# Performance work log

Hardware: AMD Instinct MI355X
Metric: run time of the kernel (lower is better)

Reference implementation:

```python
import jax, jax.numpy as jnp
import numpy as np

ALPHA = 2.0   # ATan surrogate alpha (spikingjelly default)
VTH = 0.5     # v_threshold
NUM_HEADS = 8

@jax.custom_vjp
def atan_spike(x):
    return (x >= 0.0).astype(x.dtype)

def _atan_fwd(x):
    return atan_spike(x), x

def _atan_bwd(x, g):
    return (g * (ALPHA / 2.0) / (1.0 + (jnp.pi / 2.0 * ALPHA * x) ** 2),)

atan_spike.defvjp(_atan_fwd, _atan_bwd)

def lif(x, w):
    # ParametricLIFNode, step_mode='m', decay_input=True, v_reset=0 (hard reset), detach_reset
    sg = jax.nn.sigmoid(w)
    def step(v, xt):
        v = v + (xt - v) * sg
        s = atan_spike(v - VTH)
        v = v * (1.0 - jax.lax.stop_gradient(s))  # hard reset to 0, detached
        return v, s
    _, spikes = jax.lax.scan(step, jnp.zeros_like(x[0]), x)
    return spikes

def bn_eT(x, gamma, beta, eps=1e-5):
    # x: [T, B, C, N]; per-(T,C) channel stats over (B, N)  == BatchNorm1d on [B, T*C, N] (train mode)
    T, B, C, N = x.shape
    mean = x.mean(axis=(1, 3), keepdims=True)
    var = jnp.mean((x - mean) ** 2, axis=(1, 3), keepdims=True)
    g = gamma.reshape(T, 1, C, 1)
    b = beta.reshape(T, 1, C, 1)
    return (x - mean) * jax.lax.rsqrt(var + eps) * g + b

def setup_inputs() -> dict:
    key = jax.random.key(0)
    ks = jax.random.split(key, 6)
    T, B, N, C = 16, 8, 196, 512
    return {
        "x": jax.random.normal(ks[0], (T, B, N, C), dtype=jnp.float32),
        "qkv_w": jax.random.normal(ks[1], (3 * C, C), dtype=jnp.float32) * 0.02,
        "qkv_b": jax.random.normal(ks[2], (3 * C,), dtype=jnp.float32) * 0.02,
        "bn1_g": jnp.ones((T * 3 * C,), dtype=jnp.float32),
        "bn1_b": jnp.zeros((T * 3 * C,), dtype=jnp.float32),
        "proj_w": jax.random.normal(ks[3], (C, C), dtype=jnp.float32) * 0.02,
        "proj_b": jax.random.normal(ks[4], (C,), dtype=jnp.float32) * 0.02,
        "bn2_g": jnp.ones((T * C,), dtype=jnp.float32),
        "bn2_b": jnp.zeros((T * C,), dtype=jnp.float32),
        "w_in": jnp.zeros((), dtype=jnp.float32),
        "w_q": jnp.zeros((), dtype=jnp.float32),
        "w_k": jnp.zeros((), dtype=jnp.float32),
        "w_v": jnp.zeros((), dtype=jnp.float32),
        "w_proj": jnp.zeros((), dtype=jnp.float32),
    }

def reference(x, qkv_w, qkv_b, bn1_g, bn1_b, proj_w, proj_b, bn2_g, bn2_b,
              w_in, w_q, w_k, w_v, w_proj):
    T, B, N, C = x.shape
    H = NUM_HEADS
    hd = C // H
    scale = hd ** -0.5

    x = lif(x, w_in)                                            # [T,B,N,C] spikes
    qkv = jnp.einsum('tbnc,oc->tbno', x, qkv_w) + qkv_b         # [T,B,N,3C]
    qkv = bn_eT(jnp.swapaxes(qkv, -2, -1), bn1_g, bn1_b)        # [T,B,3C,N]
    qkv = jnp.swapaxes(qkv, -2, -1).reshape(T, B, N, 3, H, hd)
    qkv = jnp.transpose(qkv, (3, 0, 1, 4, 2, 5))                # [3,T,B,H,N,hd]

    q_sk = lif(qkv[0], w_q)
    k_sk = lif(qkv[1], w_k)
    v_sk = lif(qkv[2], w_v)

    kv = jnp.einsum('tbhnd,tbhne->tbhde', k_sk, v_sk)           # k^T @ v : [T,B,H,hd,hd]
    out = jnp.einsum('tbhnd,tbhde->tbhne', q_sk, kv) * scale    # [T,B,H,N,hd]
    out = jnp.transpose(out, (0, 1, 3, 2, 4)).reshape(T, B, N, C)

    out = lif(out, w_proj)
    out = jnp.einsum('tbnc,oc->tbno', out, proj_w) + proj_b     # [T,B,N,C]
    out = bn_eT(jnp.swapaxes(out, -2, -1), bn2_g, bn2_b)        # [T,B,C,N]
    return jnp.swapaxes(out, -2, -1)                            # [T,B,N,C]
```

## Files before the change

kernel.cpp:

```cpp
#include <hip/hip_runtime.h>


#define TT 16
#define BB 8
#define NNQ 196
#define CC 512
#define HH 8
#define HD 64
#define O3 1536
#define BN (BB*NNQ)
#define PT (BN*CC)
#define WTOT ((O3+CC)*CC)
#define NRG 14

static constexpr float VTH = 0.5f;
typedef __attribute__((ext_vector_type(8))) short short8;
typedef __attribute__((ext_vector_type(4))) float f32x4;
typedef unsigned short u16;

__device__ __forceinline__ float sigm(float w){ return 1.f/(1.f+expf(-w)); }

__device__ __forceinline__ float lif_step(float x, float& v, float sg){
  float d  = __fsub_rn(x, v);
  float dd = __fmul_rn(d, sg);
  v = __fadd_rn(v, dd);
  float sp = (v >= VTH) ? 1.f : 0.f;
  v = __fmul_rn(v, __fsub_rn(1.f, sp));
  return sp;
}

__device__ __forceinline__ u16 bf16_rn(float x){
  unsigned u = __float_as_uint(x);
  unsigned r = u + 0x7FFF + ((u>>16)&1);
  return (u16)(r>>16);
}
__device__ __forceinline__ float bf16_to_f(u16 h){
  return __uint_as_float(((unsigned)h)<<16);
}

__device__ __forceinline__ void gld_lds16(const void* g, void* l){
  __builtin_amdgcn_global_load_lds(
    (const __attribute__((address_space(1))) unsigned int*)g,
    (__attribute__((address_space(3))) unsigned int*)l, 16, 0, 0);
}

__global__ void k_wsplit(const float* __restrict__ qkv_w, const float* __restrict__ proj_w,
                         u16* __restrict__ whi, u16* __restrict__ wmid, u16* __restrict__ wlo){
  int i = blockIdx.x*256 + threadIdx.x;
  float w = (i < O3*CC) ? qkv_w[i] : proj_w[i - O3*CC];
  u16 h = bf16_rn(w);          float r1 = w - bf16_to_f(h);
  u16 m = bf16_rn(r1);         float r2 = r1 - bf16_to_f(m);
  u16 l = bf16_rn(r2);
  whi[i]=h; wmid[i]=m; wlo[i]=l;
}

__global__ void k_lif_x(const float* __restrict__ x, const float* __restrict__ w,
                        float* __restrict__ vin, u16* __restrict__ s0, int t0, int tc){
  int g4 = blockIdx.x*256 + threadIdx.x;
  size_t e0 = (size_t)g4*4;
  float sg = sigm(w[0]);
  float4 v;
  if (t0==0){ v.x=0.f; v.y=0.f; v.z=0.f; v.w=0.f; }
  else v = *(const float4*)&vin[e0];
  for (int tt=0; tt<tc; ++tt){
    float4 xv = *(const float4*)&x[(size_t)(t0+tt)*PT + e0];
    ushort4 o;
    o.x = (lif_step(xv.x, v.x, sg)!=0.f) ? 0x3F80 : 0;
    o.y = (lif_step(xv.y, v.y, sg)!=0.f) ? 0x3F80 : 0;
    o.z = (lif_step(xv.z, v.z, sg)!=0.f) ? 0x3F80 : 0;
    o.w = (lif_step(xv.w, v.w, sg)!=0.f) ? 0x3F80 : 0;
    *(ushort4*)&s0[(size_t)tt*PT + e0] = o;
  }
  *(float4*)&vin[e0] = v;
}

template<int ON, int NS>
__global__ __launch_bounds__(256)
void k_gemm_mfma(const u16* __restrict__ A, const u16* __restrict__ Wh,
                 const u16* __restrict__ Wm, const u16* __restrict__ Wl,
                 const float* __restrict__ bias, float* __restrict__ Cm, int M){
  __shared__ __align__(16) u16 Al[128][64];
  __shared__ __align__(16) u16 Bs[NS][128][64];
  const u16* __restrict__ Ws[3] = {Wh, Wm, Wl};
  const int nON = ON/128;
  int nwg = gridDim.x;
  int bid = blockIdx.x;
  int q = nwg >> 3, r = nwg & 7;
  int xcd = bid & 7, idx = bid >> 3;
  int wgid = (xcd < r ? xcd*(q+1) : r*(q+1) + (xcd-r)*q) + idx;
  int mb = wgid / nON, ob = wgid - mb*nON;
  int m0 = mb*128, o0 = ob*128;

  int tid = threadIdx.x;
  int w = tid>>6, lane = tid&63;
  int wm = (w&1)*64, wn = (w>>1)*64;
  int r16 = lane&15, kg = lane>>4;
  int lrow = w*32 + (lane>>3);
  int lslot = lane&7;
  f32x4 acc[4][4] = {};
  for (int k0=0;k0<512;k0+=64){
    #pragma unroll
    for (int i=0;i<4;++i){
      int row = lrow + i*8;
      int gslot = lslot ^ (row&7);
      int gr = m0+row; if (gr>=M) gr=M-1;
      gld_lds16(&A[(size_t)gr*512 + k0 + gslot*8], &Al[w*32+i*8][0]);
      #pragma unroll
      for (int sp=0; sp<NS; ++sp)
        gld_lds16(&Ws[sp][(size_t)(o0+row)*512 + k0 + gslot*8], &Bs[sp][w*32+i*8][0]);
    }
    __syncthreads();
    #pragma unroll
    for (int s=0;s<2;++s){
      short8 af[4], bfr[NS][4];
      #pragma unroll
      for (int mt=0;mt<4;++mt){
        int rr = wm + mt*16 + r16;
        af[mt] = *(const short8*)&Al[rr][((s*4+kg)^(rr&7))*8];
      }
      #pragma unroll
      for (int nt=0;nt<4;++nt){
        int rr = wn + nt*16 + r16;
        int sl = ((s*4+kg)^(rr&7))*8;
        #pragma unroll
        for (int sp=0; sp<NS; ++sp)
          bfr[sp][nt] = *(const short8*)&Bs[sp][rr][sl];
      }
      #pragma unroll
      for (int mt=0;mt<4;++mt)
        #pragma unroll
        for (int nt=0;nt<4;++nt)
          #pragma unroll
          for (int sp=0; sp<NS; ++sp)
            acc[mt][nt] = __builtin_amdgcn_mfma_f32_16x16x32_bf16(af[mt], bfr[sp][nt], acc[mt][nt],0,0,0);
    }
    __syncthreads();
  }
  #pragma unroll
  for (int mt=0; mt<4; ++mt)
    #pragma unroll
    for (int nt=0; nt<4; ++nt){
      int o = o0 + wn + nt*16 + r16;
      float bs = bias[o];
      #pragma unroll
      for (int i=0;i<4;++i){
        int m = m0 + wm + mt*16 + kg*4 + i;
        if (m < M) Cm[(size_t)m*ON + o] = acc[mt][nt][i] + bs;
      }
    }
}

template<int O>
__global__ void k_stat_part(const float* __restrict__ X, double* __restrict__ psum,
                            double* __restrict__ psq){
  int o0 = (blockIdx.x*64 + threadIdx.x)*4;
  int tt = blockIdx.y;
  int rg = blockIdx.z;
  const float* Xb = X + (size_t)tt*BN*O;
  int r0 = rg*112;
  double s[4]={0,0,0,0}, qq[4]={0,0,0,0};
  for (int i=r0+threadIdx.y; i<r0+112; i+=4){
    float4 v = *(const float4*)&Xb[(size_t)i*O + o0];
    s[0]+=(double)v.x; qq[0]+=(double)v.x*(double)v.x;
    s[1]+=(double)v.y; qq[1]+=(double)v.y*(double)v.y;
    s[2]+=(double)v.z; qq[2]+=(double)v.z*(double)v.z;
    s[3]+=(double)v.w; qq[3]+=(double)v.w*(double)v.w;
  }
  __shared__ double ssum[4][64][4], ssq[4][64][4];
  #pragma unroll
  for (int c=0;c<4;++c){
    ssum[threadIdx.y][threadIdx.x][c]=s[c];
    ssq [threadIdx.y][threadIdx.x][c]=qq[c];
  }
  __syncthreads();
  if (threadIdx.y==0){
    #pragma unroll
    for (int c=0;c<4;++c){
      double sv = ssum[0][threadIdx.x][c]+ssum[1][threadIdx.x][c]
                + ssum[2][threadIdx.x][c]+ssum[3][threadIdx.x][c];
      double qv = ssq[0][threadIdx.x][c]+ssq[1][threadIdx.x][c]
                + ssq[2][threadIdx.x][c]+ssq[3][threadIdx.x][c];
      size_t idx = ((size_t)tt*O + o0 + c)*NRG + rg;
      psum[idx]=sv; psq[idx]=qv;
    }
  }
}

template<int O, int TCN>
__global__ void k_stat_reduce(const double* __restrict__ psum, const double* __restrict__ psq,
                              float* __restrict__ mean, float* __restrict__ rstd){
  int i = blockIdx.x*256 + threadIdx.x;
  if (i >= TCN*O) return;
  double s=0.0, q=0.0;
  #pragma unroll
  for (int g=0; g<NRG; ++g){ s += psum[(size_t)i*NRG+g]; q += psq[(size_t)i*NRG+g]; }
  double m = s*(1.0/BN);
  double var = q*(1.0/BN) - m*m;
  mean[i]=(float)m;
  rstd[i]=(float)(1.0/sqrt(var+1e-5));
}

__global__ void k_lif_qkv(const float* __restrict__ qkv, const float* __restrict__ mean,
                          const float* __restrict__ rstd, const float* __restrict__ g1,
                          const float* __restrict__ b1,
                          const float* __restrict__ wq, const float* __restrict__ wk,
                          const float* __restrict__ wv,
                          float* __restrict__ vq, float* __restrict__ vk, float* __restrict__ vv,
                          u16* __restrict__ qs, u16* __restrict__ ks,
                          u16* __restrict__ vs, int t0, int tc){
  int g4 = blockIdx.x*256 + threadIdx.x;
  int j = blockIdx.y;
  int d = (g4 & 15)*4;
  int n = (g4>>4) % NNQ;
  int h = (g4/(NNQ*16)) & 7;
  int b = g4/(NNQ*16*8);
  int o = j*CC + h*HD + d;
  const float* w = (j==0)? wq : (j==1)? wk : wv;
  float* st  = (j==0)? vq : (j==1)? vk : vv;
  u16* out = (j==0)? qs : (j==1)? ks : vs;
  float sg = sigm(w[0]);
  size_t e0 = (size_t)g4*4;
  float4 v;
  if (t0==0){ v.x=0.f; v.y=0.f; v.z=0.f; v.w=0.f; }
  else v = *(const float4*)&st[e0];
  size_t row = (size_t)(b*NNQ + n)*O3 + o;
  for (int tt=0; tt<tc; ++tt){
    float4 xv = *(const float4*)&qkv[(size_t)tt*BN*O3 + row];
    int so = tt*O3 + o;
    int go = (t0+tt)*O3 + o;
    float4 mv = *(const float4*)&mean[so];
    float4 rv = *(const float4*)&rstd[so];
    float4 gv = *(const float4*)&g1[go];
    float4 bv = *(const float4*)&b1[go];
    ushort4 ov;
    {
      float xn = __fadd_rn(__fmul_rn(__fmul_rn(__fsub_rn(xv.x, mv.x), rv.x), gv.x), bv.x);
      ov.x = (lif_step(xn, v.x, sg)!=0.f) ? 0x3F80 : 0;
    }{
      float xn = __fadd_rn(__fmul_rn(__fmul_rn(__fsub_rn(xv.y, mv.y), rv.y), gv.y), bv.y);
      ov.y = (lif_step(xn, v.y, sg)!=0.f) ? 0x3F80 : 0;
    }{
      float xn = __fadd_rn(__fmul_rn(__fmul_rn(__fsub_rn(xv.z, mv.z), rv.z), gv.z), bv.z);
      ov.z = (lif_step(xn, v.z, sg)!=0.f) ? 0x3F80 : 0;
    }{
      float xn = __fadd_rn(__fmul_rn(__fmul_rn(__fsub_rn(xv.w, mv.w), rv.w), gv.w), bv.w);
      ov.w = (lif_step(xn, v.w, sg)!=0.f) ? 0x3F80 : 0;
    }
    *(ushort4*)&out[(size_t)tt*PT + e0] = ov;
  }
  *(float4*)&st[e0] = v;
}

__global__ __launch_bounds__(256)
void k_kvqv_mfma(const u16* __restrict__ ks, const u16* __restrict__ vs,
                 const u16* __restrict__ qs, float* __restrict__ attn){
  __shared__ __align__(16) u16 Kb[224][64];
  __shared__ __align__(16) u16 Vb[224][64];
  __shared__ __align__(16) u16 kvb[64][64];
  int blk = blockIdx.x;
  size_t base = (size_t)blk * (NNQ*HD);
  int tid = threadIdx.x, w = tid>>6, lane = tid&63;
  int r16 = lane&15, kg = lane>>4;
  for (int u=tid; u<224*8; u+=256){
    int row=u>>3, slot=u&7;
    int sl = slot ^ (((row>>3)&3)<<1);
    float4 z = {0.f,0.f,0.f,0.f};
    float4 kd = z, vd = z;
    if (row < NNQ){
      kd = *(const float4*)&ks[base + (size_t)row*64 + slot*8];
      vd = *(const float4*)&vs[base + (size_t)row*64 + slot*8];
    }
    *(float4*)&Kb[row][sl*8] = kd;
    *(float4*)&Vb[row][sl*8] = vd;
  }
  __syncthreads();
  f32x4 acc[4] = {};
  int d0 = w*16;
  for (int n0=0;n0<224;n0+=32){
    int sw = (((n0 + kg*8)>>3)&3)<<4;
    short8 af;
    #pragma unroll
    for (int jj=0;jj<8;++jj) af[jj] = (short)Kb[n0+kg*8+jj][(d0 + r16) ^ sw];
    #pragma unroll
    for (int nt=0;nt<4;++nt){
      short8 bf;
      #pragma unroll
      for (int jj=0;jj<8;++jj) bf[jj] = (short)Vb[n0+kg*8+jj][(nt*16 + r16) ^ sw];
      acc[nt] = __builtin_amdgcn_mfma_f32_16x16x32_bf16(af, bf, acc[nt],0,0,0);
    }
  }
  #pragma unroll
  for (int nt=0;nt<4;++nt)
    #pragma unroll
    for (int i=0;i<4;++i){
      int d = d0 + kg*4 + i;
      kvb[d][(nt*16 + r16) ^ (((d>>3)&3)<<4)] = (u16)(__float_as_uint(acc[nt][i])>>16);
    }
  __syncthreads();
  for (int u=tid; u<224*8; u+=256){
    int row=u>>3, slot=u&7;
    int sl = slot ^ (row&7);
    float4 qd = {0.f,0.f,0.f,0.f};
    if (row < NNQ) qd = *(const float4*)&qs[base + (size_t)row*64 + slot*8];
    *(float4*)&Kb[row][sl*8] = qd;
  }
  __syncthreads();
  short8 bkv[2][4];
  #pragma unroll
  for (int s=0;s<2;++s){
    int sw2 = ((s*4 + kg)&3)<<4;
    #pragma unroll
    for (int nt=0;nt<4;++nt){
      short8 bf;
      #pragma unroll
      for (int jj=0;jj<8;++jj) bf[jj] = (short)kvb[s*32 + kg*8 + jj][(nt*16 + r16) ^ sw2];
      bkv[s][nt] = bf;
    }
  }
  for (int mt=w; mt<13; mt+=4){
    f32x4 a2[4] = {};
    short8 qa[2];
    #pragma unroll
    for (int s=0;s<2;++s){
      int rr = mt*16 + r16;
      qa[s] = *(const short8*)&Kb[rr][(((s*4+kg)^(rr&7)))*8];
    }
    #pragma unroll
    for (int s=0;s<2;++s)
      #pragma unroll
      for (int nt=0;nt<4;++nt)
        a2[nt] = __builtin_amdgcn_mfma_f32_16x16x32_bf16(qa[s], bkv[s][nt], a2[nt],0,0,0);
    #pragma unroll
    for (int nt=0;nt<4;++nt){
      int e = nt*16 + r16;
      #pragma unroll
      for (int i=0;i<4;++i){
        int n = mt*16 + kg*4 + i;
        if (n < NNQ) attn[base + (size_t)n*64 + e] = a2[nt][i]*0.125f;
      }
    }
  }
}

__global__ void k_lif_attn(const float* __restrict__ ain, const float* __restrict__ w,
                           float* __restrict__ vo, u16* __restrict__ sp, int t0, int tc){
  int g4 = blockIdx.x*256 + threadIdx.x;
  int e = (g4 & 15)*4;
  int n = (g4>>4) % NNQ;
  int h = (g4/(NNQ*16)) & 7;
  int b = g4/(NNQ*16*8);
  size_t e0 = (size_t)g4*4;
  size_t dst = (size_t)(b*NNQ + n)*CC + h*HD + e;
  float sg = sigm(w[0]);
  float4 v;
  if (t0==0){ v.x=0.f; v.y=0.f; v.z=0.f; v.w=0.f; }
  else v = *(const float4*)&vo[e0];
  for (int tt=0; tt<tc; ++tt){
    float4 xv = *(const float4*)&ain[(size_t)tt*PT + e0];
    ushort4 ov;
    ov.x = (lif_step(xv.x, v.x, sg)!=0.f) ? 0x3F80 : 0;
    ov.y = (lif_step(xv.y, v.y, sg)!=0.f) ? 0x3F80 : 0;
    ov.z = (lif_step(xv.z, v.z, sg)!=0.f) ? 0x3F80 : 0;
    ov.w = (lif_step(xv.w, v.w, sg)!=0.f) ? 0x3F80 : 0;
    *(ushort4*)&sp[(size_t)tt*PT + dst] = ov;
  }
  *(float4*)&vo[e0] = v;
}

__global__ void k_bn2_apply(float* __restrict__ Y, const float* __restrict__ mean,
                            const float* __restrict__ rstd, const float* __restrict__ g2,
                            const float* __restrict__ b2, int t0){
  size_t idx = ((size_t)blockIdx.x*256 + threadIdx.x)*4;
  int tt = (int)(idx / PT);
  size_t off = idx - (size_t)tt*PT;
  int c = (int)(off & (CC-1));
  float4 xv = *(const float4*)&Y[idx];
  float4 mv = *(const float4*)&mean[tt*CC + c];
  float4 rv = *(const float4*)&rstd[tt*CC + c];
  float4 gv = *(const float4*)&g2[(t0+tt)*CC + c];
  float4 bv = *(const float4*)&b2[(t0+tt)*CC + c];
  float4 yv;
  yv.x = __fadd_rn(__fmul_rn(__fmul_rn(__fsub_rn(xv.x, mv.x), rv.x), gv.x), bv.x);
  yv.y = __fadd_rn(__fmul_rn(__fmul_rn(__fsub_rn(xv.y, mv.y), rv.y), gv.y), bv.y);
  yv.z = __fadd_rn(__fmul_rn(__fmul_rn(__fsub_rn(xv.z, mv.z), rv.z), gv.z), bv.z);
  yv.w = __fadd_rn(__fmul_rn(__fmul_rn(__fsub_rn(xv.w, mv.w), rv.w), gv.w), bv.w);
  *(float4*)&Y[idx] = yv;
}

extern "C" void kernel_launch(void* const* d_in, const int* in_sizes, int n_in,
                              void* d_out, int out_size, void* d_ws, size_t ws_size,
                              hipStream_t stream){
  const float* x      = (const float*)d_in[0];
  const float* qkv_w  = (const float*)d_in[1];
  const float* qkv_b  = (const float*)d_in[2];
  const float* bn1_g  = (const float*)d_in[3];
  const float* bn1_b  = (const float*)d_in[4];
  const float* proj_w = (const float*)d_in[5];
  const float* proj_b = (const float*)d_in[6];
  const float* bn2_g  = (const float*)d_in[7];
  const float* bn2_b  = (const float*)d_in[8];
  const float* w_in   = (const float*)d_in[9];
  const float* w_q    = (const float*)d_in[10];
  const float* w_k    = (const float*)d_in[11];
  const float* w_v    = (const float*)d_in[12];
  const float* w_proj = (const float*)d_in[13];
  float* outp = (float*)d_out;

  auto need = [](int tc)->size_t{
    return 4ull*5*PT + 8ull*tc*O3 + 8ull*tc*CC
         + 16ull*tc*O3*NRG + 16ull*tc*CC*NRG
         + 6ull*WTOT
         + 10ull*tc*PT
         + 4ull*tc*BN*O3;
  };
  int TC = 16;
  while (TC > 1 && need(TC) > ws_size) TC >>= 1;

  char* p = (char*)d_ws;
  float* vin = (float*)p; p += 4ull*PT;
  float* vq  = (float*)p; p += 4ull*PT;
  float* vk  = (float*)p; p += 4ull*PT;
  float* vv  = (float*)p; p += 4ull*PT;
  float* vo  = (float*)p; p += 4ull*PT;
  float* mean1 = (float*)p; p += 4ull*TC*O3;
  float* rstd1 = (float*)p; p += 4ull*TC*O3;
  float* mean2 = (float*)p; p += 4ull*TC*CC;
  float* rstd2 = (float*)p; p += 4ull*TC*CC;
  double* p1sum = (double*)p; p += 8ull*TC*O3*NRG;
  double* p1sq  = (double*)p; p += 8ull*TC*O3*NRG;
  double* p2sum = (double*)p; p += 8ull*TC*CC*NRG;
  double* p2sq  = (double*)p; p += 8ull*TC*CC*NRG;
  u16* whi  = (u16*)p; p += 2ull*WTOT;
  u16* wmid = (u16*)p; p += 2ull*WTOT;
  u16* wlo  = (u16*)p; p += 2ull*WTOT;
  u16* s0    = (u16*)p; p += 2ull*TC*PT;
  u16* qsb   = (u16*)p; p += 2ull*TC*PT;
  u16* ksb   = (u16*)p; p += 2ull*TC*PT;
  u16* vsb   = (u16*)p; p += 2ull*TC*PT;
  u16* sproj = (u16*)p; p += 2ull*TC*PT;
  float* qkv_all = (float*)p;
  float* attn    = qkv_all;

  k_wsplit<<<WTOT/256, 256, 0, stream>>>(qkv_w, proj_w, whi, wmid, wlo);

  for (int t0=0; t0<TT; t0+=TC){
    int M = TC*BN;
    int nMB = (M+127)/128;
    float* outc = outp + (size_t)t0*PT;
    k_lif_x<<<PT/1024, 256, 0, stream>>>(x, w_in, vin, s0, t0, TC);

    k_gemm_mfma<O3,3><<<nMB*(O3/128), 256, 0, stream>>>(
        s0, whi, wmid, wlo, qkv_b, qkv_all, M);

    k_stat_part<O3><<<dim3(O3/256, TC, NRG), dim3(64,4), 0, stream>>>(qkv_all, p1sum, p1sq);
    if (TC == 16)
      k_stat_reduce<O3,16><<<(16*O3+255)/256, 256, 0, stream>>>(p1sum, p1sq, mean1, rstd1);
    else if (TC == 8)
      k_stat_reduce<O3,8><<<(8*O3+255)/256, 256, 0, stream>>>(p1sum, p1sq, mean1, rstd1);
    else
      k_stat_reduce<O3,4><<<(4*O3+255)/256, 256, 0, stream>>>(p1sum, p1sq, mean1, rstd1);

    k_lif_qkv<<<dim3(PT/1024, 3), 256, 0, stream>>>(qkv_all, mean1, rstd1, bn1_g, bn1_b,
                                                    w_q, w_k, w_v, vq, vk, vv,
                                                    qsb, ksb, vsb, t0, TC);

    k_kvqv_mfma<<<TC*BB*HH, 256, 0, stream>>>(ksb, vsb, qsb, attn);

    k_lif_attn<<<PT/1024, 256, 0, stream>>>(attn, w_proj, vo, sproj, t0, TC);

    k_gemm_mfma<CC,2><<<nMB*(CC/128), 256, 0, stream>>>(
        sproj, whi + (size_t)O3*CC, wmid + (size_t)O3*CC, wlo + (size_t)O3*CC,
        proj_b, outc, M);

    k_stat_part<CC><<<dim3(CC/256, TC, NRG), dim3(64,4), 0, stream>>>(outc, p2sum, p2sq);
    if (TC == 16)
      k_stat_reduce<CC,16><<<(16*CC+255)/256, 256, 0, stream>>>(p2sum, p2sq, mean2, rstd2);
    else if (TC == 8)
      k_stat_reduce<CC,8><<<(8*CC+255)/256, 256, 0, stream>>>(p2sum, p2sq, mean2, rstd2);
    else
      k_stat_reduce<CC,4><<<(4*CC+255)/256, 256, 0, stream>>>(p2sum, p2sq, mean2, rstd2);

    k_bn2_apply<<<(TC*(size_t)PT)/1024, 256, 0, stream>>>(outc, mean2, rstd2,
                                                          bn2_g, bn2_b, t0);
  }
}
```

Before: 373.5 us.

## Transpose K/V into LDS for vector fragment loads and prefetch Q to registers

K and V tiles are now written into shared memory transposed (d-major, XOR-swizzled), so each MFMA A/B fragment becomes one 16-byte LDS read instead of eight scalar reads. The kv intermediate is stored transposed with a padded stride, which also turns its fragment loads into vector reads. Q is loaded from global memory into registers at kernel start, so its latency overlaps the K/V phase. The costs are scalar 2-byte LDS stores during the transpose and extra register pressure from the 7 float4 Q prefetch buffers.

```diff
diff --git a/kernel.cpp b/kernel.cpp
--- a/kernel.cpp
+++ b/kernel.cpp
@@ -254,76 +254,93 @@
 __global__ __launch_bounds__(256)
 void k_kvqv_mfma(const u16* __restrict__ ks, const u16* __restrict__ vs,
                  const u16* __restrict__ qs, float* __restrict__ attn){
-  __shared__ __align__(16) u16 Kb[224][64];
-  __shared__ __align__(16) u16 Vb[224][64];
-  __shared__ __align__(16) u16 kvb[64][64];
+  __shared__ __align__(16) u16 Kt[64*256];
+  __shared__ __align__(16) u16 Vt[64*256];
+  __shared__ __align__(16) u16 kvbT[64*72];
   int blk = blockIdx.x;
   size_t base = (size_t)blk * (NNQ*HD);
   int tid = threadIdx.x, w = tid>>6, lane = tid&63;
   int r16 = lane&15, kg = lane>>4;
+
+  float4 qreg[7];
+  #pragma unroll
+  for (int i=0;i<7;++i){
+    int u = tid + i*256;
+    int row = u>>3, slot = u&7;
+    float4 qd = {0.f,0.f,0.f,0.f};
+    if (row < NNQ) qd = *(const float4*)&qs[base + (size_t)row*64 + slot*8];
+    qreg[i] = qd;
+  }
+
   for (int u=tid; u<224*8; u+=256){
-    int row=u>>3, slot=u&7;
-    int sl = slot ^ (((row>>3)&3)<<1);
-    float4 z = {0.f,0.f,0.f,0.f};
-    float4 kd = z, vd = z;
-    if (row < NNQ){
-      kd = *(const float4*)&ks[base + (size_t)row*64 + slot*8];
-      vd = *(const float4*)&vs[base + (size_t)row*64 + slot*8];
-    }
-    *(float4*)&Kb[row][sl*8] = kd;
-    *(float4*)&Vb[row][sl*8] = vd;
+    int n = u>>3, dsl = u&7;
+    float4 kd = {0.f,0.f,0.f,0.f}, vd = kd;
+    if (n < NNQ){
+      kd = *(const float4*)&ks[base + (size_t)n*64 + dsl*8];
+      vd = *(const float4*)&vs[base + (size_t)n*64 + dsl*8];
+    }
+    const u16* kp = (const u16*)&kd;
+    const u16* vp = (const u16*)&vd;
+    int nslot = n>>3, nin = n&7;
+    #pragma unroll
+    for (int jj=0;jj<8;++jj){
+      int d = dsl*8 + jj;
+      int col = ((nslot ^ (d&7))<<3) + nin;
+      Kt[d*256 + col] = kp[jj];
+      Vt[d*256 + col] = vp[jj];
+    }
   }
   __syncthreads();
+
   f32x4 acc[4] = {};
   int d0 = w*16;
+  int dA = d0 + r16;
   for (int n0=0;n0<224;n0+=32){
-    int sw = (((n0 + kg*8)>>3)&3)<<4;
-    short8 af;
-    #pragma unroll
-    for (int jj=0;jj<8;++jj) af[jj] = (short)Kb[n0+kg*8+jj][(d0 + r16) ^ sw];
+    int cb = (n0>>3) + kg;
+    short8 af = *(const short8*)&Kt[dA*256 + ((cb ^ (dA&7))<<3)];
     #pragma unroll
     for (int nt=0;nt<4;++nt){
-      short8 bf;
-      #pragma unroll
-      for (int jj=0;jj<8;++jj) bf[jj] = (short)Vb[n0+kg*8+jj][(nt*16 + r16) ^ sw];
+      int eB = nt*16 + r16;
+      short8 bf = *(const short8*)&Vt[eB*256 + ((cb ^ (eB&7))<<3)];
       acc[nt] = __builtin_amdgcn_mfma_f32_16x16x32_bf16(af, bf, acc[nt],0,0,0);
     }
   }
   #pragma unroll
-  for (int nt=0;nt<4;++nt)
+  for (int nt=0;nt<4;++nt){
+    int e = nt*16 + r16;
     #pragma unroll
     for (int i=0;i<4;++i){
       int d = d0 + kg*4 + i;
-      kvb[d][(nt*16 + r16) ^ (((d>>3)&3)<<4)] = (u16)(__float_as_uint(acc[nt][i])>>16);
-    }
+      kvbT[e*72 + d] = (u16)(__float_as_uint(acc[nt][i])>>16);
+    }
+  }
   __syncthreads();
-  for (int u=tid; u<224*8; u+=256){
-    int row=u>>3, slot=u&7;
+
+  u16* Qb = &Kt[0];
+  #pragma unroll
+  for (int i=0;i<7;++i){
+    int u = tid + i*256;
+    int row = u>>3, slot = u&7;
     int sl = slot ^ (row&7);
-    float4 qd = {0.f,0.f,0.f,0.f};
-    if (row < NNQ) qd = *(const float4*)&qs[base + (size_t)row*64 + slot*8];
-    *(float4*)&Kb[row][sl*8] = qd;
+    *(float4*)&Qb[row*64 + sl*8] = qreg[i];
   }
   __syncthreads();
+
   short8 bkv[2][4];
   #pragma unroll
-  for (int s=0;s<2;++s){
-    int sw2 = ((s*4 + kg)&3)<<4;
+  for (int s=0;s<2;++s)
     #pragma unroll
     for (int nt=0;nt<4;++nt){
-      short8 bf;
-      #pragma unroll
-      for (int jj=0;jj<8;++jj) bf[jj] = (short)kvb[s*32 + kg*8 + jj][(nt*16 + r16) ^ sw2];
-      bkv[s][nt] = bf;
-    }
-  }
+      int e = nt*16 + r16;
+      bkv[s][nt] = *(const short8*)&kvbT[e*72 + s*32 + kg*8];
+    }
   for (int mt=w; mt<13; mt+=4){
     f32x4 a2[4] = {};
     short8 qa[2];
     #pragma unroll
     for (int s=0;s<2;++s){
       int rr = mt*16 + r16;
-      qa[s] = *(const short8*)&Kb[rr][(((s*4+kg)^(rr&7)))*8];
+      qa[s] = *(const short8*)&Qb[rr*64 + (((s*4+kg)^(rr&7)))*8];
     }
     #pragma unroll
     for (int s=0;s<2;++s)
```

Result: no change. 380.1 us (+1.8%).

## Halve LDS footprint in kv/qv kernel by chunking K/V and reading Q directly

Applied to the files above, without the earlier changes.

The K/V staging buffers shrink from 224 to 128 rows, and the N dimension is processed in two chunks (128 rows, then 96 rows) with a sync between them. The kv result is stored transposed with a new swizzle so each B-fragment becomes a single 16-byte LDS read instead of eight scalar reads. Q fragments are loaded straight from global memory rather than staged through LDS, with a clamped row index for padding rows. This lowers shared memory per block to raise occupancy and cuts LDS traffic, at the cost of an extra barrier and uncoalesced-ish global Q loads.

```diff
diff --git a/kernel.cpp b/kernel.cpp
--- a/kernel.cpp
+++ b/kernel.cpp
@@ -254,29 +254,26 @@
 __global__ __launch_bounds__(256)
 void k_kvqv_mfma(const u16* __restrict__ ks, const u16* __restrict__ vs,
                  const u16* __restrict__ qs, float* __restrict__ attn){
-  __shared__ __align__(16) u16 Kb[224][64];
-  __shared__ __align__(16) u16 Vb[224][64];
+  __shared__ __align__(16) u16 Kb[128][64];
+  __shared__ __align__(16) u16 Vb[128][64];
   __shared__ __align__(16) u16 kvb[64][64];
   int blk = blockIdx.x;
   size_t base = (size_t)blk * (NNQ*HD);
   int tid = threadIdx.x, w = tid>>6, lane = tid&63;
   int r16 = lane&15, kg = lane>>4;
-  for (int u=tid; u<224*8; u+=256){
+  f32x4 acc[4] = {};
+  int d0 = w*16;
+
+  for (int u=tid; u<128*8; u+=256){
     int row=u>>3, slot=u&7;
     int sl = slot ^ (((row>>3)&3)<<1);
-    float4 z = {0.f,0.f,0.f,0.f};
-    float4 kd = z, vd = z;
-    if (row < NNQ){
-      kd = *(const float4*)&ks[base + (size_t)row*64 + slot*8];
-      vd = *(const float4*)&vs[base + (size_t)row*64 + slot*8];
-    }
+    float4 kd = *(const float4*)&ks[base + (size_t)row*64 + slot*8];
+    float4 vd = *(const float4*)&vs[base + (size_t)row*64 + slot*8];
     *(float4*)&Kb[row][sl*8] = kd;
     *(float4*)&Vb[row][sl*8] = vd;
   }
   __syncthreads();
-  f32x4 acc[4] = {};
-  int d0 = w*16;
-  for (int n0=0;n0<224;n0+=32){
+  for (int n0=0;n0<128;n0+=32){
     int sw = (((n0 + kg*8)>>3)&3)<<4;
     short8 af;
     #pragma unroll
@@ -289,42 +286,59 @@
       acc[nt] = __builtin_amdgcn_mfma_f32_16x16x32_bf16(af, bf, acc[nt],0,0,0);
     }
   }
+  __syncthreads();
+  for (int u=tid; u<96*8; u+=256){
+    int row=u>>3, slot=u&7;
+    int g = row + 128;
+    int sl = slot ^ (((row>>3)&3)<<1);
+    float4 kd = {0.f,0.f,0.f,0.f}, vd = kd;
+    if (g < NNQ){
+      kd = *(const float4*)&ks[base + (size_t)g*64 + slot*8];
+      vd = *(const float4*)&vs[base + (size_t)g*64 + slot*8];
+    }
+    *(float4*)&Kb[row][sl*8] = kd;
+    *(float4*)&Vb[row][sl*8] = vd;
+  }
+  __syncthreads();
+  for (int n0=0;n0<96;n0+=32){
+    int sw = (((n0 + kg*8)>>3)&3)<<4;
+    short8 af;
+    #pragma unroll
+    for (int jj=0;jj<8;++jj) af[jj] = (short)Kb[n0+kg*8+jj][(d0 + r16) ^ sw];
+    #pragma unroll
+    for (int nt=0;nt<4;++nt){
+      short8 bf;
+      #pragma unroll
+      for (int jj=0;jj<8;++jj) bf[jj] = (short)Vb[n0+kg*8+jj][(nt*16 + r16) ^ sw];
+      acc[nt] = __builtin_amdgcn_mfma_f32_16x16x32_bf16(af, bf, acc[nt],0,0,0);
+    }
+  }
   #pragma unroll
-  for (int nt=0;nt<4;++nt)
+  for (int nt=0;nt<4;++nt){
+    int e = nt*16 + r16;
     #pragma unroll
     for (int i=0;i<4;++i){
       int d = d0 + kg*4 + i;
-      kvb[d][(nt*16 + r16) ^ (((d>>3)&3)<<4)] = (u16)(__float_as_uint(acc[nt][i])>>16);
-    }
-  __syncthreads();
-  for (int u=tid; u<224*8; u+=256){
-    int row=u>>3, slot=u&7;
-    int sl = slot ^ (row&7);
-    float4 qd = {0.f,0.f,0.f,0.f};
-    if (row < NNQ) qd = *(const float4*)&qs[base + (size_t)row*64 + slot*8];
-    *(float4*)&Kb[row][sl*8] = qd;
+      kvb[e][d ^ ((e&7)<<3)] = (u16)(__float_as_uint(acc[nt][i])>>16);
+    }
   }
   __syncthreads();
   short8 bkv[2][4];
   #pragma unroll
-  for (int s=0;s<2;++s){
-    int sw2 = ((s*4 + kg)&3)<<4;
+  for (int s=0;s<2;++s)
     #pragma unroll
     for (int nt=0;nt<4;++nt){
-      short8 bf;
-      #pragma unroll
-      for (int jj=0;jj<8;++jj) bf[jj] = (short)kvb[s*32 + kg*8 + jj][(nt*16 + r16) ^ sw2];
-      bkv[s][nt] = bf;
-    }
-  }
+      int e = nt*16 + r16;
+      bkv[s][nt] = *(const short8*)&kvb[e][(s*32 + kg*8) ^ ((e&7)<<3)];
+    }
   for (int mt=w; mt<13; mt+=4){
     f32x4 a2[4] = {};
     short8 qa[2];
-    #pragma unroll
-    for (int s=0;s<2;++s){
-      int rr = mt*16 + r16;
-      qa[s] = *(const short8*)&Kb[rr][(((s*4+kg)^(rr&7)))*8];
-    }
+    int rr = mt*16 + r16;
+    int rc = (rr < NNQ) ? rr : (NNQ-1);
+    #pragma unroll
+    for (int s=0;s<2;++s)
+      qa[s] = *(const short8*)&qs[base + (size_t)rc*64 + s*32 + kg*8];
     #pragma unroll
     for (int s=0;s<2;++s)
       #pragma unroll
```

Measured after the change: 375.2 us. No clear change (+0.5%).
